# Kernel tuning notes

Measured on AMD Instinct MI355X. Metric: run time of the kernel, lower is better.

## Reference

```python
import jax, jax.numpy as jnp
import numpy as np

# surrogate-gradient spike (multi-gaussian, standard DH-SNN act_fun_adp constants)
GAMMA, LENS, SCALE, HIGHT = 0.5, 0.5, 6.0, 0.15
B_J0, BETA_ADAPT, VTH = 1.6, 1.8, 1.0
IN_DIM, N1, N2, OUT_DIM, BRANCH = 76, 50, 100, 2, 4
BATCH, SEQ = 256, 1000

def _gauss(x, mu, sigma):
    return jnp.exp(-((x - mu) ** 2) / (2.0 * sigma ** 2)) / (jnp.sqrt(2.0 * jnp.pi) * sigma)

@jax.custom_vjp
def spike_fn(x):
    return (x > 0).astype(x.dtype)

def _spike_fwd(x):
    return spike_fn(x), x

def _spike_bwd(x, g):
    sg = (_gauss(x, 0.0, LENS) * (1.0 + HIGHT)
          - _gauss(x, LENS, SCALE * LENS) * HIGHT
          - _gauss(x, -LENS, SCALE * LENS) * HIGHT)
    return (g * sg * GAMMA,)

spike_fn.defvjp(_spike_fwd, _spike_bwd)

def branch_mask(in_dim, out_dim, branch):
    # each dendritic branch k sees contiguous chunk k of the (input|recurrent) vector
    isize = in_dim + out_dim
    seg = int(np.ceil(isize / branch))
    m = np.zeros((out_dim * branch, isize), np.float32)
    for k in range(branch):
        m[k::branch, k * seg:min((k + 1) * seg, isize)] = 1.0
    return jnp.asarray(m)

def setup_inputs():
    key = jax.random.key(0)
    ks = jax.random.split(key, 12)
    def lin(k, o, i):
        lim = 1.0 / np.sqrt(i)
        kw, kb = jax.random.split(k)
        return (jax.random.uniform(kw, (o, i), jnp.float32, -lim, lim),
                jax.random.uniform(kb, (o,), jnp.float32, -lim, lim))
    W1, b1 = lin(ks[0], N1 * BRANCH, IN_DIM + N1)
    W2, b2 = lin(ks[1], N2 * BRANCH, N1 + N2)
    Wx, bx = lin(ks[2], N2, 2 * N2)
    Wm, bm = lin(ks[3], N2, 2 * N2)
    Wa, ba = lin(ks[4], N2, 2 * N2)
    Wd = jax.random.normal(ks[5], (OUT_DIM, N2), jnp.float32) * np.sqrt(2.0 / (OUT_DIM + N2))
    bd = jnp.zeros((OUT_DIM,), jnp.float32)
    tau_m1 = jax.random.uniform(ks[6], (N1,), jnp.float32, 0.0, 4.0)
    tau_n1 = jax.random.uniform(ks[7], (N1, BRANCH), jnp.float32, 0.0, 4.0)
    tau_m2 = jax.random.uniform(ks[8], (N2,), jnp.float32, 0.0, 4.0)
    tau_n2 = jax.random.uniform(ks[9], (N2, BRANCH), jnp.float32, 0.0, 4.0)
    tau_md = jax.random.uniform(ks[10], (OUT_DIM,), jnp.float32, 0.0, 4.0)
    x = jax.random.normal(ks[11], (BATCH, SEQ, IN_DIM), jnp.float32)
    return dict(x=x, W1=W1, b1=b1, tau_m1=tau_m1, tau_n1=tau_n1,
                W2=W2, b2=b2, tau_m2=tau_m2, tau_n2=tau_n2,
                Wx=Wx, bx=bx, Wm=Wm, bm=bm, Wa=Wa, ba=ba,
                Wd=Wd, bd=bd, tau_md=tau_md)

def _denri_step(xt, mem, spk, d, W, b, tau_m, tau_n, n_out):
    # dendritic spiking neuron (spike_rnn_test_denri_wotanh_R)
    kin = jnp.concatenate([xt, spk], axis=1)                       # [B, in+out]
    beta = jax.nn.sigmoid(tau_n)                                   # [out, branch]
    proj = (kin @ W.T + b).reshape(-1, n_out, BRANCH)              # [B, out, branch]
    d = beta * d + (1.0 - beta) * proj
    alpha = jax.nn.sigmoid(tau_m)
    mem = mem * alpha + (1.0 - alpha) * d.sum(-1) - VTH * spk
    spk = spike_fn(mem - VTH)
    return mem, spk, d

def _liquid_step(xt, mem, spk, bth, Wx, bx, Wm, bm, Wa, ba):
    # liquid time-constant adaptive-threshold cell (SNN_rec_cell, is_rec=True)
    dx = jnp.concatenate([xt, spk], axis=1) @ Wx.T + bx
    tauM = jax.nn.sigmoid(jnp.concatenate([dx, mem], axis=1) @ Wm.T + bm)
    tauA = jax.nn.sigmoid(jnp.concatenate([dx, bth], axis=1) @ Wa.T + ba)
    bth = tauA * bth + (1.0 - tauA) * spk
    B = B_J0 + BETA_ADAPT * bth
    mem = mem * tauM + (1.0 - tauM) * dx - B * spk
    spk = spike_fn(mem - B)
    return mem, spk, bth

def reference(x, W1, b1, tau_m1, tau_n1, W2, b2, tau_m2, tau_n2,
              Wx, bx, Wm, bm, Wa, ba, Wd, bd, tau_md):
    Bsz = x.shape[0]
    W1m = W1 * branch_mask(IN_DIM, N1, BRANCH)
    W2m = W2 * branch_mask(N1, N2, BRANCH)
    alpha_d = jax.nn.sigmoid(tau_md)
    z = lambda *s: jnp.zeros(s, x.dtype)
    carry0 = (z(Bsz, N1), z(Bsz, N1), z(Bsz, N1, BRANCH),
              z(Bsz, N2), z(Bsz, N2), z(Bsz, N2, BRANCH),
              z(Bsz, N2), z(Bsz, N2), jnp.full((Bsz, N2), B_J0, x.dtype),
              z(Bsz, OUT_DIM))

    def step(carry, xt):
        m1, s1, d1, m2, s2, d2, lm, ls, lb, md = carry
        m1, s1, d1 = _denri_step(xt, m1, s1, d1, W1m, b1, tau_m1, tau_n1, N1)
        m2, s2, d2 = _denri_step(s1, m2, s2, d2, W2m, b2, tau_m2, tau_n2, N2)
        # original detaches the liquid hidden tuple every step
        lm, ls, lb = (jax.lax.stop_gradient(t) for t in (lm, ls, lb))
        lm, ls, lb = _liquid_step(s2, lm, ls, lb, Wx, bx, Wm, bm, Wa, ba)
        md = md * alpha_d + (1.0 - alpha_d) * (ls @ Wd.T + bd)    # readout integrator
        return (m1, s1, d1, m2, s2, d2, lm, ls, lb, md), md

    _, md_seq = jax.lax.scan(step, carry0, jnp.swapaxes(x, 0, 1))  # [T, B, OUT]
    return md_seq[1:].sum(axis=0)  # output only accumulated for i > 0
```

## Files before the change

kernel.cpp:

```cpp
#include <hip/hip_runtime.h>
#include <math.h>

#define SEQ 1000
#define IND 76
#define PIDX(i) ((((i)/25)*28) + ((i)%25))

__device__ __forceinline__ float sigf(float v) { return 1.0f / (1.0f + expf(-v)); }

__global__ void pack_w2(const float* __restrict__ W2, float* __restrict__ w2pk) {
    const int i = blockIdx.x * 256 + threadIdx.x;
    if (i >= 400 * 40) return;
    const int r = i / 40, u = i - 40 * r;
    const int col = 38 * (r & 3) + u;
    w2pk[i] = (u < 38 && col < 150) ? W2[r * 150 + col] : 0.f;
}

__global__ void pack_wx(const float* __restrict__ Wx, float* __restrict__ wxpk) {
    const int i = blockIdx.x * 256 + threadIdx.x;
    if (i >= 2 * 200 * 64) return;
    const int p = i / (200 * 64);
    const int rem = i - p * 200 * 64;
    const int s = rem / 64, u = rem - 64 * s;
    const int g = s >> 2, c = s & 3;
    const int j = (u >= 28) ? 1 : 0;
    const int local = u - 28 * j;
    float v = 0.f;
    if (local < 25) {
        const int col = (p == 0 ? 100 : 0) + 25 * c + local;
        v = Wx[(2 * g + j) * 200 + col];
    }
    wxpk[i] = v;
}

__global__ __launch_bounds__(512) void dhsnn_fwd(
    const float* __restrict__ x,
    const float* __restrict__ W1, const float* __restrict__ b1,
    const float* __restrict__ tau_m1, const float* __restrict__ tau_n1,
    const float* __restrict__ b2, const float* __restrict__ tau_m2,
    const float* __restrict__ tau_n2,
    const float* __restrict__ bxp, const float* __restrict__ bm,
    const float* __restrict__ ba,
    const float* __restrict__ Wm, const float* __restrict__ Wa,
    const float* __restrict__ Wd, const float* __restrict__ bd,
    const float* __restrict__ tau_md,
    const float* __restrict__ w2pk, const float* __restrict__ wxpk,
    float* __restrict__ out)
{
    const int t   = (int)threadIdx.x;
    const int blk = (int)blockIdx.x;

    __shared__ __align__(16) float kin1P[128];
    __shared__ __align__(16) float kin2P[4][40];
    __shared__ __align__(16) float s2P[112];
    __shared__ __align__(16) float dxP[112];
    __shared__ __align__(16) float lsP[112];
    __shared__ __align__(16) float lmP[112];
    __shared__ __align__(16) float lbP[112];
    __shared__ __align__(16) float sEarly[200];
    __shared__ __align__(16) float dxEarly[100];
    __shared__ __align__(16) float rpart[200];
    __shared__ __align__(16) float r2[8];
    __shared__ float b2S[400], bt2S[400], al2S[100], bmS[100], baS[100], bxS[100];
    __shared__ float wdS[200], b1S[200], bt1S[200], al1S[50];

    for (int i = t; i < 128; i += 512) kin1P[i] = 0.f;
    for (int i = t; i < 160; i += 512) (&kin2P[0][0])[i] = 0.f;
    for (int i = t; i < 112; i += 512) { s2P[i]=0.f; dxP[i]=0.f; lsP[i]=0.f; lmP[i]=0.f; lbP[i]=0.f; }
    for (int i = t; i < 200; i += 512) { sEarly[i] = 0.f; rpart[i] = 0.f; }
    for (int i = t; i < 100; i += 512) dxEarly[i] = 0.f;
    if (t < 8) r2[t] = 0.f;
    if (t < 400) { b2S[t] = b2[t]; bt2S[t] = sigf(tau_n2[t]); }
    if (t < 100) { al2S[t] = sigf(tau_m2[t]); bmS[t] = bm[t]; baS[t] = ba[t]; bxS[t] = bxp[t]; }
    if (t < 200) { wdS[t] = Wd[(t < 100 ? 0 : 100) + (t % 100)];
                   b1S[t] = b1[t]; bt1S[t] = sigf(tau_n1[t]); }
    if (t < 50)  al1S[t] = sigf(tau_m1[t]);

    const int c     = t & 3;
    const int lbase = (t & 63) & ~3;

    float wreg[100];
    float pA = 0.f, pB = 0.f, pC = 0.f, pD = 0.f;
    float mA = 0.f, mS = 0.f;
    float4 xq0 = make_float4(0,0,0,0), xq1 = make_float4(0,0,0,0);

    if (t < 400) {
        const bool late = (t >= 200);
        const int  sg   = late ? ((t - 200) >> 2) : (t >> 2);
        const int  colb = (late ? 0 : 100) + 25 * c;
        const int  r0 = 2 * sg, r1 = 2 * sg + 1;
        #pragma unroll
        for (int u = 0; u < 25; ++u) {
            wreg[u]      = Wm[r0 * 200 + colb + u];
            wreg[25 + u] = Wm[r1 * 200 + colb + u];
            wreg[50 + u] = Wa[r0 * 200 + colb + u];
            wreg[75 + u] = Wa[r1 * 200 + colb + u];
        }
    } else if (t < 500) {
        const int m = t - 400;
        const int rA_ = 2 * m, rB_ = 2 * m + 1;
        const int kA = rA_ & 3, kB = rB_ & 3;
        #pragma unroll
        for (int u = 0; u < 32; ++u) {
            const int cA = 32 * kA + u, cB = 32 * kB + u;
            wreg[u]      = (cA < 126) ? W1[rA_ * 126 + cA] : 0.f;
            wreg[32 + u] = (cB < 126) ? W1[rB_ * 126 + cB] : 0.f;
        }
    } else if (t == 508 || t == 509) {
        pC = sigf(tau_md[t - 508]);
        pD = bd[t - 508];
    }

    auto l1_step = [&]() {
        const int m = t - 400;
        const float* a0p = kin1P + 32 * ((2 * m) & 3);
        const float* a1p = kin1P + 32 * ((2 * m + 1) & 3);
        float acc0 = b1S[2 * m], acc1 = b1S[2 * m + 1];
        #pragma unroll
        for (int u4 = 0; u4 < 8; ++u4) {
            const float4 av = *reinterpret_cast<const float4*>(a0p + 4 * u4);
            acc0 = fmaf(wreg[4*u4+0], av.x, acc0); acc0 = fmaf(wreg[4*u4+1], av.y, acc0);
            acc0 = fmaf(wreg[4*u4+2], av.z, acc0); acc0 = fmaf(wreg[4*u4+3], av.w, acc0);
        }
        #pragma unroll
        for (int u4 = 0; u4 < 8; ++u4) {
            const float4 av = *reinterpret_cast<const float4*>(a1p + 4 * u4);
            acc1 = fmaf(wreg[32+4*u4+0], av.x, acc1); acc1 = fmaf(wreg[32+4*u4+1], av.y, acc1);
            acc1 = fmaf(wreg[32+4*u4+2], av.z, acc1); acc1 = fmaf(wreg[32+4*u4+3], av.w, acc1);
        }
        const float b0 = bt1S[2 * m], b1v = bt1S[2 * m + 1];
        pC = b0 * pC + (1.f - b0) * acc0;
        pD = b1v * pD + (1.f - b1v) * acc1;
        const float pCo = __shfl(pC, (t & 63) | 1, 64);
        const float pDo = __shfl(pD, (t & 63) | 1, 64);
        if ((t & 1) == 0) {
            const float sum = ((pC + pD) + pCo) + pDo;
            const float al = al1S[m >> 1];
            mA = al * mA + (1.f - al) * sum - mS;
            mS = (mA - 1.0f > 0.f) ? 1.f : 0.f;
        }
    };

    __syncthreads();
    if (t < 100) lbP[PIDX(t)] = 1.6f;
    if (t >= 500) {
        const int i0 = t - 500;
        const float* xb = x + (size_t)blk * SEQ * IND;
        *reinterpret_cast<float4*>(&kin1P[4 * i0]) =
            *reinterpret_cast<const float4*>(xb + 4 * i0);
        if (i0 < 7)
            *reinterpret_cast<float4*>(&kin1P[4 * (i0 + 12)]) =
                *reinterpret_cast<const float4*>(xb + 4 * (i0 + 12));
    }
    __syncthreads();
    if (t >= 400 && t < 500) l1_step();
    __syncthreads();
    if (t >= 400 && t < 500 && (t & 1) == 0) {
        const int n = (t - 400) >> 1;
        kin1P[76 + n] = mS;
        const int w = (n >= 38) ? 1 : 0;
        kin2P[w][n - 38 * w] = mS;
    }
    if (t >= 500) {
        const int i0 = t - 500;
        const float* xb = x + ((size_t)blk * SEQ + 1) * IND;
        *reinterpret_cast<float4*>(&kin1P[4 * i0]) =
            *reinterpret_cast<const float4*>(xb + 4 * i0);
        if (i0 < 7)
            *reinterpret_cast<float4*>(&kin1P[4 * (i0 + 12)]) =
                *reinterpret_cast<const float4*>(xb + 4 * (i0 + 12));
    }
    __syncthreads();

    for (int j = 0; j < SEQ; ++j) {
        if (t < 400) {
            const float4* wrow = reinterpret_cast<const float4*>(w2pk + t * 40);
            const float* kw = kin2P[c];
            float a0=0.f, a1=0.f, a2=0.f, a3=0.f;
            #pragma unroll
            for (int cc = 0; cc < 10; ++cc) {
                const float4 wv = wrow[cc];
                const float4 av = *reinterpret_cast<const float4*>(kw + 4 * cc);
                a0 = fmaf(wv.x, av.x, a0); a1 = fmaf(wv.y, av.y, a1);
                a2 = fmaf(wv.z, av.z, a2); a3 = fmaf(wv.w, av.w, a3);
            }
            const float proj = b2S[t] + ((a0 + a1) + (a2 + a3));
            const float bt = bt2S[t];
            pA = bt * pA + (1.f - bt) * proj;
            const float d1 = __shfl(pA, lbase + 1, 64);
            const float d2 = __shfl(pA, lbase + 2, 64);
            const float d3 = __shfl(pA, lbase + 3, 64);
            if (c == 0) {
                const int q = t >> 2;
                const float al = al2S[q];
                const float sum = ((pA + d1) + d2) + d3;
                pB = al * pB + (1.f - al) * sum - s2P[PIDX(q)];
                s2P[PIDX(q)] = (pB - 1.0f > 0.f) ? 1.f : 0.f;
            }
        }
        if (t < 200) {
            const int g = t >> 2;
            {
                const float* apM = lmP + 28 * c;
                const float* apA = lbP + 28 * c;
                float P0=0.f, P1=0.f, P2=0.f, P3=0.f;
                #pragma unroll
                for (int u4 = 0; u4 < 6; ++u4) {
                    const float4 am = *reinterpret_cast<const float4*>(apM + 4 * u4);
                    const float4 aa = *reinterpret_cast<const float4*>(apA + 4 * u4);
                    P0 = fmaf(wreg[   4*u4+0], am.x, P0); P0 = fmaf(wreg[   4*u4+1], am.y, P0);
                    P0 = fmaf(wreg[   4*u4+2], am.z, P0); P0 = fmaf(wreg[   4*u4+3], am.w, P0);
                    P1 = fmaf(wreg[25+4*u4+0], am.x, P1); P1 = fmaf(wreg[25+4*u4+1], am.y, P1);
                    P1 = fmaf(wreg[25+4*u4+2], am.z, P1); P1 = fmaf(wreg[25+4*u4+3], am.w, P1);
                    P2 = fmaf(wreg[50+4*u4+0], aa.x, P2); P2 = fmaf(wreg[50+4*u4+1], aa.y, P2);
                    P2 = fmaf(wreg[50+4*u4+2], aa.z, P2); P2 = fmaf(wreg[50+4*u4+3], aa.w, P2);
                    P3 = fmaf(wreg[75+4*u4+0], aa.x, P3); P3 = fmaf(wreg[75+4*u4+1], aa.y, P3);
                    P3 = fmaf(wreg[75+4*u4+2], aa.z, P3); P3 = fmaf(wreg[75+4*u4+3], aa.w, P3);
                }
                P0 = fmaf(wreg[24], apM[24], P0); P1 = fmaf(wreg[49], apM[24], P1);
                P2 = fmaf(wreg[74], apA[24], P2); P3 = fmaf(wreg[99], apA[24], P3);
                float Q0 = P0 + __shfl_xor(P0, 1, 64), Q1 = P1 + __shfl_xor(P1, 1, 64);
                float Q2 = P2 + __shfl_xor(P2, 1, 64), Q3 = P3 + __shfl_xor(P3, 1, 64);
                float R0 = Q0 + __shfl_xor(Q0, 2, 64), R1 = Q1 + __shfl_xor(Q1, 2, 64);
                float R2 = Q2 + __shfl_xor(Q2, 2, 64), R3 = Q3 + __shfl_xor(Q3, 2, 64);
                sEarly[t] = (c == 0) ? R0 : (c == 1) ? R1 : (c == 2) ? R2 : R3;
            }
            {
                const float* wE = wxpk + (size_t)t * 64;
                const float* aq = lsP + 28 * c;
                float f0 = 0.f, f1 = 0.f;
                #pragma unroll
                for (int u4 = 0; u4 < 6; ++u4) {
                    const float4 w0v = *reinterpret_cast<const float4*>(wE + 4 * u4);
                    const float4 w1v = *reinterpret_cast<const float4*>(wE + 28 + 4 * u4);
                    const float4 av  = *reinterpret_cast<const float4*>(aq + 4 * u4);
                    f0 = fmaf(w0v.x, av.x, f0); f0 = fmaf(w0v.y, av.y, f0);
                    f0 = fmaf(w0v.z, av.z, f0); f0 = fmaf(w0v.w, av.w, f0);
                    f1 = fmaf(w1v.x, av.x, f1); f1 = fmaf(w1v.y, av.y, f1);
                    f1 = fmaf(w1v.z, av.z, f1); f1 = fmaf(w1v.w, av.w, f1);
                }
                f0 = fmaf(wE[24], aq[24], f0);
                f1 = fmaf(wE[52], aq[24], f1);
                float Qf0 = f0 + __shfl_xor(f0, 1, 64), Qf1 = f1 + __shfl_xor(f1, 1, 64);
                float Rf0 = Qf0 + __shfl_xor(Qf0, 2, 64), Rf1 = Qf1 + __shfl_xor(Qf1, 2, 64);
                if (c == 0) dxEarly[2 * g] = Rf0;
                else if (c == 1) dxEarly[2 * g + 1] = Rf1;
            }
            rpart[t] = wdS[t] * lsP[PIDX(t - (t < 100 ? 0 : 100))];
        } else if (t >= 400 && t < 500) {
            if (j < SEQ - 1) l1_step();
        } else if (t >= 500) {
            if (j + 2 < SEQ) {
                const int i0 = t - 500;
                const float* xb = x + ((size_t)blk * SEQ + (j + 2)) * IND;
                xq0 = *reinterpret_cast<const float4*>(xb + 4 * i0);
                if (i0 < 7) xq1 = *reinterpret_cast<const float4*>(xb + 4 * (i0 + 12));
            }
        }
        __syncthreads();
        if (t >= 200 && t < 400) {
            const int s = t - 200, g = s >> 2;
            const float* wL = wxpk + (size_t)(200 + s) * 64;
            const float* aq = s2P + 28 * c;
            float f0 = 0.f, f1 = 0.f;
            #pragma unroll
            for (int u4 = 0; u4 < 6; ++u4) {
                const float4 w0v = *reinterpret_cast<const float4*>(wL + 4 * u4);
                const float4 w1v = *reinterpret_cast<const float4*>(wL + 28 + 4 * u4);
                const float4 av  = *reinterpret_cast<const float4*>(aq + 4 * u4);
                f0 = fmaf(w0v.x, av.x, f0); f0 = fmaf(w0v.y, av.y, f0);
                f0 = fmaf(w0v.z, av.z, f0); f0 = fmaf(w0v.w, av.w, f0);
                f1 = fmaf(w1v.x, av.x, f1); f1 = fmaf(w1v.y, av.y, f1);
                f1 = fmaf(w1v.z, av.z, f1); f1 = fmaf(w1v.w, av.w, f1);
            }
            f0 = fmaf(wL[24], aq[24], f0);
            f1 = fmaf(wL[52], aq[24], f1);
            float Qf0 = f0 + __shfl_xor(f0, 1, 64), Qf1 = f1 + __shfl_xor(f1, 1, 64);
            float Rf0 = Qf0 + __shfl_xor(Qf0, 2, 64), Rf1 = Qf1 + __shfl_xor(Qf1, 2, 64);
            if (c == 0)      dxP[PIDX(2 * g)]     = (Rf0 + dxEarly[2 * g])     + bxS[2 * g];
            else if (c == 1) dxP[PIDX(2 * g + 1)] = (Rf1 + dxEarly[2 * g + 1]) + bxS[2 * g + 1];
        } else if (t < 200) {
            if (c == 0) {
                const int q = t >> 2;
                const int col = 50 + q;
                const int w = (col >= 114) ? 3 : ((col >= 76) ? 2 : 1);
                kin2P[w][col - 38 * w] = s2P[PIDX(q)];
            }
        } else if (t >= 500) {
            if (t < 508) {
                const int rr = t - 500;
                float sV = 0.f;
                #pragma unroll
                for (int u = 0; u < 25; ++u) sV += rpart[25 * rr + u];
                r2[rr] = sV;
            }
            if (j + 2 < SEQ) {
                const int i0 = t - 500;
                *reinterpret_cast<float4*>(&kin1P[4 * i0]) = xq0;
                if (i0 < 7) *reinterpret_cast<float4*>(&kin1P[4 * (i0 + 12)]) = xq1;
            }
        }
        if (t >= 200 && t < 400 && c == 0) {
            const int q = t >> 2;
            const int col = 50 + q;
            const int w = (col >= 114) ? 3 : ((col >= 76) ? 2 : 1);
            kin2P[w][col - 38 * w] = s2P[PIDX(q)];
        }
        __syncthreads();
        if (t >= 200 && t < 400) {
            const int s = t - 200, g = s >> 2;
            const float* apD = dxP + 28 * c;
            float P0=0.f, P1=0.f, P2=0.f, P3=0.f;
            #pragma unroll
            for (int u4 = 0; u4 < 6; ++u4) {
                const float4 ad = *reinterpret_cast<const float4*>(apD + 4 * u4);
                P0 = fmaf(wreg[   4*u4+0], ad.x, P0); P0 = fmaf(wreg[   4*u4+1], ad.y, P0);
                P0 = fmaf(wreg[   4*u4+2], ad.z, P0); P0 = fmaf(wreg[   4*u4+3], ad.w, P0);
                P1 = fmaf(wreg[25+4*u4+0], ad.x, P1); P1 = fmaf(wreg[25+4*u4+1], ad.y, P1);
                P1 = fmaf(wreg[25+4*u4+2], ad.z, P1); P1 = fmaf(wreg[25+4*u4+3], ad.w, P1);
                P2 = fmaf(wreg[50+4*u4+0], ad.x, P2); P2 = fmaf(wreg[50+4*u4+1], ad.y, P2);
                P2 = fmaf(wreg[50+4*u4+2], ad.z, P2); P2 = fmaf(wreg[50+4*u4+3], ad.w, P2);
                P3 = fmaf(wreg[75+4*u4+0], ad.x, P3); P3 = fmaf(wreg[75+4*u4+1], ad.y, P3);
                P3 = fmaf(wreg[75+4*u4+2], ad.z, P3); P3 = fmaf(wreg[75+4*u4+3], ad.w, P3);
            }
            P0 = fmaf(wreg[24], apD[24], P0); P1 = fmaf(wreg[49], apD[24], P1);
            P2 = fmaf(wreg[74], apD[24], P2); P3 = fmaf(wreg[99], apD[24], P3);
            float Q0 = P0 + __shfl_xor(P0, 1, 64), Q1 = P1 + __shfl_xor(P1, 1, 64);
            float Q2 = P2 + __shfl_xor(P2, 1, 64), Q3 = P3 + __shfl_xor(P3, 1, 64);
            float R0 = Q0 + __shfl_xor(Q0, 2, 64), R1 = Q1 + __shfl_xor(Q1, 2, 64);
            float R2 = Q2 + __shfl_xor(Q2, 2, 64), R3 = Q3 + __shfl_xor(Q3, 2, 64);
            const float sel  = (c == 0) ? R0 : (c == 1) ? R1 : (c == 2) ? R2 : R3;
            const float bias = (c < 2) ? bmS[2 * g + c] : baS[2 * g + c - 2];
            const float tv = sigf((sel + sEarly[s]) + bias);
            const float taP = __shfl(tv, lbase + 2 + (c & 1), 64);
            if (c < 2) {
                const int rq = 2 * g + c;
                const float lm = lmP[PIDX(rq)], lb = lbP[PIDX(rq)];
                const float ls = lsP[PIDX(rq)], dxv = dxP[PIDX(rq)];
                const float lbN = taP * lb + (1.f - taP) * ls;
                const float Bv  = 1.6f + 1.8f * lbN;
                const float lmN = lm * tv + (1.f - tv) * dxv - Bv * ls;
                const float lsN = (lmN - Bv > 0.f) ? 1.f : 0.f;
                lmP[PIDX(rq)] = lmN; lbP[PIDX(rq)] = lbN; lsP[PIDX(rq)] = lsN;
            }
        } else if (t >= 400 && t < 500) {
            if ((t & 1) == 0 && j < SEQ - 1) {
                const int n = (t - 400) >> 1;
                kin1P[76 + n] = mS;
                const int w = (n >= 38) ? 1 : 0;
                kin2P[w][n - 38 * w] = mS;
            }
        } else if ((t == 508 || t == 509) && j >= 1) {
            const int o = t - 508;
            const float dot = ((r2[4*o] + r2[4*o+1]) + (r2[4*o+2] + r2[4*o+3])) + pD;
            mA = pC * mA + (1.f - pC) * dot;
            if (j >= 2) mS += mA;
        }
        __syncthreads();
    }

    if (t < 200) rpart[t] = wdS[t] * lsP[PIDX(t - (t < 100 ? 0 : 100))];
    __syncthreads();
    if (t >= 500 && t < 508) {
        const int rr = t - 500;
        float sV = 0.f;
        #pragma unroll
        for (int u = 0; u < 25; ++u) sV += rpart[25 * rr + u];
        r2[rr] = sV;
    }
    __syncthreads();
    if (t == 508 || t == 509) {
        const int o = t - 508;
        const float dot = ((r2[4*o] + r2[4*o+1]) + (r2[4*o+2] + r2[4*o+3])) + pD;
        mA = pC * mA + (1.f - pC) * dot;
        mS += mA;
        out[blk * 2 + o] = mS;
    }
}

extern "C" void kernel_launch(void* const* d_in, const int* in_sizes, int n_in,
                              void* d_out, int out_size, void* d_ws, size_t ws_size,
                              hipStream_t stream) {
    const float* x      = (const float*)d_in[0];
    const float* W1     = (const float*)d_in[1];
    const float* b1     = (const float*)d_in[2];
    const float* tau_m1 = (const float*)d_in[3];
    const float* tau_n1 = (const float*)d_in[4];
    const float* W2     = (const float*)d_in[5];
    const float* b2     = (const float*)d_in[6];
    const float* tau_m2 = (const float*)d_in[7];
    const float* tau_n2 = (const float*)d_in[8];
    const float* Wx     = (const float*)d_in[9];
    const float* bx     = (const float*)d_in[10];
    const float* Wm     = (const float*)d_in[11];
    const float* bm     = (const float*)d_in[12];
    const float* Wa     = (const float*)d_in[13];
    const float* ba     = (const float*)d_in[14];
    const float* Wd     = (const float*)d_in[15];
    const float* bd     = (const float*)d_in[16];
    const float* tau_md = (const float*)d_in[17];
    float* out  = (float*)d_out;
    float* w2pk = (float*)d_ws;
    float* wxpk = (float*)d_ws + 16000;

    pack_w2<<<(400 * 40 + 255) / 256, 256, 0, stream>>>(W2, w2pk);
    pack_wx<<<(2 * 200 * 64 + 255) / 256, 256, 0, stream>>>(Wx, wxpk);

    const int batch = in_sizes[0] / (SEQ * IND);
    dhsnn_fwd<<<batch, 512, 0, stream>>>(x, W1, b1, tau_m1, tau_n1,
                                         b2, tau_m2, tau_n2,
                                         bx, bm, ba, Wm, Wa,
                                         Wd, bd, tau_md,
                                         w2pk, wxpk, out);
}
```

Before: 4.713 ms.

## Software-pipeline layer-2 with double-buffered inputs to cut per-step barriers

Double-buffers the layer-1 and layer-2 input vectors so layer 2 runs one step ahead on 200 threads (two rows each), overlapping with the liquid-layer update. Both Wx partial products (early and late) now run in one phase, and the readout reduction is done with wave shuffles instead of a shared r2 buffer. Together these drop each timestep from three barriers to two, shortening the serial critical path. The cost is more per-thread work for the layer-2 threads and more intricate buffer-parity logic, which could introduce off-by-one timing errors.

```diff
diff --git a/kernel.cpp b/kernel.cpp
--- a/kernel.cpp
+++ b/kernel.cpp
@@ -49,38 +49,33 @@
     const int t   = (int)threadIdx.x;
     const int blk = (int)blockIdx.x;
 
-    __shared__ __align__(16) float kin1P[128];
-    __shared__ __align__(16) float kin2P[4][40];
+    __shared__ __align__(16) float kin1B[2][128];
+    __shared__ __align__(16) float kin2B[2][4][40];
     __shared__ __align__(16) float s2P[112];
     __shared__ __align__(16) float dxP[112];
     __shared__ __align__(16) float lsP[112];
     __shared__ __align__(16) float lmP[112];
     __shared__ __align__(16) float lbP[112];
     __shared__ __align__(16) float sEarly[200];
-    __shared__ __align__(16) float dxEarly[100];
     __shared__ __align__(16) float rpart[200];
-    __shared__ __align__(16) float r2[8];
     __shared__ float b2S[400], bt2S[400], al2S[100], bmS[100], baS[100], bxS[100];
     __shared__ float wdS[200], b1S[200], bt1S[200], al1S[50];
 
-    for (int i = t; i < 128; i += 512) kin1P[i] = 0.f;
-    for (int i = t; i < 160; i += 512) (&kin2P[0][0])[i] = 0.f;
+    for (int i = t; i < 256; i += 512) (&kin1B[0][0])[i] = 0.f;
+    for (int i = t; i < 320; i += 512) (&kin2B[0][0][0])[i] = 0.f;
     for (int i = t; i < 112; i += 512) { s2P[i]=0.f; dxP[i]=0.f; lsP[i]=0.f; lmP[i]=0.f; lbP[i]=0.f; }
     for (int i = t; i < 200; i += 512) { sEarly[i] = 0.f; rpart[i] = 0.f; }
-    for (int i = t; i < 100; i += 512) dxEarly[i] = 0.f;
-    if (t < 8) r2[t] = 0.f;
     if (t < 400) { b2S[t] = b2[t]; bt2S[t] = sigf(tau_n2[t]); }
     if (t < 100) { al2S[t] = sigf(tau_m2[t]); bmS[t] = bm[t]; baS[t] = ba[t]; bxS[t] = bxp[t]; }
     if (t < 200) { wdS[t] = Wd[(t < 100 ? 0 : 100) + (t % 100)];
                    b1S[t] = b1[t]; bt1S[t] = sigf(tau_n1[t]); }
     if (t < 50)  al1S[t] = sigf(tau_m1[t]);
 
-    const int c     = t & 3;
-    const int lbase = (t & 63) & ~3;
+    const int c = t & 3;
 
     float wreg[100];
-    float pA = 0.f, pB = 0.f, pC = 0.f, pD = 0.f;
-    float mA = 0.f, mS = 0.f;
+    float pA = 0.f, pB = 0.f, pD = 0.f, pS = 0.f;
+    float mdA = 0.f, mdB = 0.f;
     float4 xq0 = make_float4(0,0,0,0), xq1 = make_float4(0,0,0,0);
 
     if (t < 400) {
@@ -106,14 +101,14 @@
             wreg[32 + u] = (cB < 126) ? W1[rB_ * 126 + cB] : 0.f;
         }
     } else if (t == 508 || t == 509) {
-        pC = sigf(tau_md[t - 508]);
-        pD = bd[t - 508];
-    }
-
-    auto l1_step = [&]() {
+        mdA = sigf(tau_md[t - 508]);
+        mdB = bd[t - 508];
+    }
+
+    auto l1_step = [&](int p) {
         const int m = t - 400;
-        const float* a0p = kin1P + 32 * ((2 * m) & 3);
-        const float* a1p = kin1P + 32 * ((2 * m + 1) & 3);
+        const float* a0p = kin1B[p] + 32 * ((2 * m) & 3);
+        const float* a1p = kin1B[p] + 32 * ((2 * m + 1) & 3);
         float acc0 = b1S[2 * m], acc1 = b1S[2 * m + 1];
         #pragma unroll
         for (int u4 = 0; u4 < 8; ++u4) {
@@ -128,15 +123,65 @@
             acc1 = fmaf(wreg[32+4*u4+2], av.z, acc1); acc1 = fmaf(wreg[32+4*u4+3], av.w, acc1);
         }
         const float b0 = bt1S[2 * m], b1v = bt1S[2 * m + 1];
-        pC = b0 * pC + (1.f - b0) * acc0;
+        pA = b0 * pA + (1.f - b0) * acc0;
         pD = b1v * pD + (1.f - b1v) * acc1;
-        const float pCo = __shfl(pC, (t & 63) | 1, 64);
+        const float pAo = __shfl(pA, (t & 63) | 1, 64);
         const float pDo = __shfl(pD, (t & 63) | 1, 64);
         if ((t & 1) == 0) {
-            const float sum = ((pC + pD) + pCo) + pDo;
+            const float sum = ((pA + pD) + pAo) + pDo;
             const float al = al1S[m >> 1];
-            mA = al * mA + (1.f - al) * sum - mS;
-            mS = (mA - 1.0f > 0.f) ? 1.f : 0.f;
+            pB = al * pB + (1.f - al) * sum - pS;
+            pS = (pB - 1.0f > 0.f) ? 1.f : 0.f;
+        }
+    };
+    auto s1_write = [&](int pk1, int pk2) {
+        const int n = (t - 400) >> 1;
+        kin1B[pk1][76 + n] = pS;
+        const int w = (n >= 38) ? 1 : 0;
+        kin2B[pk2][w][n - 38 * w] = pS;
+    };
+
+    auto l2_step = [&](int p, int p2) {
+        const int r0 = 2 * t, r1 = r0 + 1;
+        const float4* w0 = reinterpret_cast<const float4*>(w2pk + r0 * 40);
+        const float4* w1 = reinterpret_cast<const float4*>(w2pk + r1 * 40);
+        const float* k0 = kin2B[p][r0 & 3];
+        const float* k1 = kin2B[p][r1 & 3];
+        float a0=0.f, a1=0.f, a2=0.f, a3=0.f;
+        #pragma unroll
+        for (int cc = 0; cc < 10; ++cc) {
+            const float4 wv = w0[cc];
+            const float4 av = *reinterpret_cast<const float4*>(k0 + 4 * cc);
+            a0 = fmaf(wv.x, av.x, a0); a1 = fmaf(wv.y, av.y, a1);
+            a2 = fmaf(wv.z, av.z, a2); a3 = fmaf(wv.w, av.w, a3);
+        }
+        __builtin_amdgcn_sched_barrier(0);
+        float b0=0.f, b1v=0.f, b2v=0.f, b3=0.f;
+        #pragma unroll
+        for (int cc = 0; cc < 10; ++cc) {
+            const float4 wv = w1[cc];
+            const float4 av = *reinterpret_cast<const float4*>(k1 + 4 * cc);
+            b0 = fmaf(wv.x, av.x, b0); b1v = fmaf(wv.y, av.y, b1v);
+            b2v = fmaf(wv.z, av.z, b2v); b3 = fmaf(wv.w, av.w, b3);
+        }
+        const float proj0 = b2S[r0] + ((a0 + a1) + (a2 + a3));
+        const float bt0 = bt2S[r0];
+        pA = bt0 * pA + (1.f - bt0) * proj0;
+        const float proj1 = b2S[r1] + ((b0 + b1v) + (b2v + b3));
+        const float bt1v = bt2S[r1];
+        pD = bt1v * pD + (1.f - bt1v) * proj1;
+        const float sA = __shfl(pA, (t & 63) | 1, 64);
+        const float sD = __shfl(pD, (t & 63) | 1, 64);
+        if ((t & 1) == 0) {
+            const int q = t >> 1;
+            const float sum = ((pA + pD) + sA) + sD;
+            const float al = al2S[q];
+            pB = al * pB + (1.f - al) * sum - s2P[PIDX(q)];
+            const float s2n = (pB - 1.0f > 0.f) ? 1.f : 0.f;
+            s2P[PIDX(q)] = s2n;
+            const int col = 50 + q;
+            const int w = (col >= 114) ? 3 : ((col >= 76) ? 2 : 1);
+            kin2B[p2][w][col - 38 * w] = s2n;
         }
     };
 
@@ -145,61 +190,34 @@
     if (t >= 500) {
         const int i0 = t - 500;
         const float* xb = x + (size_t)blk * SEQ * IND;
-        *reinterpret_cast<float4*>(&kin1P[4 * i0]) =
+        *reinterpret_cast<float4*>(&kin1B[0][4 * i0]) =
             *reinterpret_cast<const float4*>(xb + 4 * i0);
         if (i0 < 7)
-            *reinterpret_cast<float4*>(&kin1P[4 * (i0 + 12)]) =
+            *reinterpret_cast<float4*>(&kin1B[0][4 * (i0 + 12)]) =
                 *reinterpret_cast<const float4*>(xb + 4 * (i0 + 12));
     }
     __syncthreads();
-    if (t >= 400 && t < 500) l1_step();
-    __syncthreads();
-    if (t >= 400 && t < 500 && (t & 1) == 0) {
-        const int n = (t - 400) >> 1;
-        kin1P[76 + n] = mS;
-        const int w = (n >= 38) ? 1 : 0;
-        kin2P[w][n - 38 * w] = mS;
-    }
-    if (t >= 500) {
+    if (t >= 400 && t < 500) {
+        l1_step(0);
+        if ((t & 1) == 0) s1_write(1, 0);
+    } else if (t >= 500) {
         const int i0 = t - 500;
         const float* xb = x + ((size_t)blk * SEQ + 1) * IND;
-        *reinterpret_cast<float4*>(&kin1P[4 * i0]) =
+        *reinterpret_cast<float4*>(&kin1B[1][4 * i0]) =
             *reinterpret_cast<const float4*>(xb + 4 * i0);
         if (i0 < 7)
-            *reinterpret_cast<float4*>(&kin1P[4 * (i0 + 12)]) =
+            *reinterpret_cast<float4*>(&kin1B[1][4 * (i0 + 12)]) =
                 *reinterpret_cast<const float4*>(xb + 4 * (i0 + 12));
     }
     __syncthreads();
+    if (t < 200) l2_step(0, 1);
+    __syncthreads();
 
     for (int j = 0; j < SEQ; ++j) {
-        if (t < 400) {
-            const float4* wrow = reinterpret_cast<const float4*>(w2pk + t * 40);
-            const float* kw = kin2P[c];
-            float a0=0.f, a1=0.f, a2=0.f, a3=0.f;
-            #pragma unroll
-            for (int cc = 0; cc < 10; ++cc) {
-                const float4 wv = wrow[cc];
-                const float4 av = *reinterpret_cast<const float4*>(kw + 4 * cc);
-                a0 = fmaf(wv.x, av.x, a0); a1 = fmaf(wv.y, av.y, a1);
-                a2 = fmaf(wv.z, av.z, a2); a3 = fmaf(wv.w, av.w, a3);
-            }
-            const float proj = b2S[t] + ((a0 + a1) + (a2 + a3));
-            const float bt = bt2S[t];
-            pA = bt * pA + (1.f - bt) * proj;
-            const float d1 = __shfl(pA, lbase + 1, 64);
-            const float d2 = __shfl(pA, lbase + 2, 64);
-            const float d3 = __shfl(pA, lbase + 3, 64);
-            if (c == 0) {
-                const int q = t >> 2;
-                const float al = al2S[q];
-                const float sum = ((pA + d1) + d2) + d3;
-                pB = al * pB + (1.f - al) * sum - s2P[PIDX(q)];
-                s2P[PIDX(q)] = (pB - 1.0f > 0.f) ? 1.f : 0.f;
-            }
-        }
+        const int pj1 = (j + 1) & 1, pj0 = j & 1;
         if (t < 200) {
-            const int g = t >> 2;
             {
+                const int g = t >> 2;  (void)g;
                 const float* apM = lmP + 28 * c;
                 const float* apA = lbP + 28 * c;
                 float P0=0.f, P1=0.f, P2=0.f, P3=0.f;
@@ -224,31 +242,52 @@
                 float R2 = Q2 + __shfl_xor(Q2, 2, 64), R3 = Q3 + __shfl_xor(Q3, 2, 64);
                 sEarly[t] = (c == 0) ? R0 : (c == 1) ? R1 : (c == 2) ? R2 : R3;
             }
-            {
-                const float* wE = wxpk + (size_t)t * 64;
-                const float* aq = lsP + 28 * c;
-                float f0 = 0.f, f1 = 0.f;
-                #pragma unroll
-                for (int u4 = 0; u4 < 6; ++u4) {
-                    const float4 w0v = *reinterpret_cast<const float4*>(wE + 4 * u4);
-                    const float4 w1v = *reinterpret_cast<const float4*>(wE + 28 + 4 * u4);
-                    const float4 av  = *reinterpret_cast<const float4*>(aq + 4 * u4);
-                    f0 = fmaf(w0v.x, av.x, f0); f0 = fmaf(w0v.y, av.y, f0);
-                    f0 = fmaf(w0v.z, av.z, f0); f0 = fmaf(w0v.w, av.w, f0);
-                    f1 = fmaf(w1v.x, av.x, f1); f1 = fmaf(w1v.y, av.y, f1);
-                    f1 = fmaf(w1v.z, av.z, f1); f1 = fmaf(w1v.w, av.w, f1);
-                }
-                f0 = fmaf(wE[24], aq[24], f0);
-                f1 = fmaf(wE[52], aq[24], f1);
-                float Qf0 = f0 + __shfl_xor(f0, 1, 64), Qf1 = f1 + __shfl_xor(f1, 1, 64);
-                float Rf0 = Qf0 + __shfl_xor(Qf0, 2, 64), Rf1 = Qf1 + __shfl_xor(Qf1, 2, 64);
-                if (c == 0) dxEarly[2 * g] = Rf0;
-                else if (c == 1) dxEarly[2 * g + 1] = Rf1;
-            }
-            rpart[t] = wdS[t] * lsP[PIDX(t - (t < 100 ? 0 : 100))];
-        } else if (t >= 400 && t < 500) {
-            if (j < SEQ - 1) l1_step();
-        } else if (t >= 500) {
+            rpart[t] = wdS[t] * lsP[PIDX(t % 100)];
+        } else if (t < 400) {
+            const int s = t - 200, g = s >> 2;
+            const float* wEp = wxpk + (size_t)s * 64;
+            const float* wLp = wxpk + (size_t)(200 + s) * 64;
+            const float* aE = lsP + 28 * c;
+            const float* aL = s2P + 28 * c;
+            float e0=0.f, e1=0.f;
+            #pragma unroll
+            for (int u4 = 0; u4 < 6; ++u4) {
+                const float4 w0v = *reinterpret_cast<const float4*>(wEp + 4 * u4);
+                const float4 w1v = *reinterpret_cast<const float4*>(wEp + 28 + 4 * u4);
+                const float4 av  = *reinterpret_cast<const float4*>(aE + 4 * u4);
+                e0 = fmaf(w0v.x, av.x, e0); e0 = fmaf(w0v.y, av.y, e0);
+                e0 = fmaf(w0v.z, av.z, e0); e0 = fmaf(w0v.w, av.w, e0);
+                e1 = fmaf(w1v.x, av.x, e1); e1 = fmaf(w1v.y, av.y, e1);
+                e1 = fmaf(w1v.z, av.z, e1); e1 = fmaf(w1v.w, av.w, e1);
+            }
+            e0 = fmaf(wEp[24], aE[24], e0);
+            e1 = fmaf(wEp[52], aE[24], e1);
+            __builtin_amdgcn_sched_barrier(0);
+            float l0=0.f, l1v=0.f;
+            #pragma unroll
+            for (int u4 = 0; u4 < 6; ++u4) {
+                const float4 w0v = *reinterpret_cast<const float4*>(wLp + 4 * u4);
+                const float4 w1v = *reinterpret_cast<const float4*>(wLp + 28 + 4 * u4);
+                const float4 av  = *reinterpret_cast<const float4*>(aL + 4 * u4);
+                l0 = fmaf(w0v.x, av.x, l0); l0 = fmaf(w0v.y, av.y, l0);
+                l0 = fmaf(w0v.z, av.z, l0); l0 = fmaf(w0v.w, av.w, l0);
+                l1v = fmaf(w1v.x, av.x, l1v); l1v = fmaf(w1v.y, av.y, l1v);
+                l1v = fmaf(w1v.z, av.z, l1v); l1v = fmaf(w1v.w, av.w, l1v);
+            }
+            l0  = fmaf(wLp[24], aL[24], l0);
+            l1v = fmaf(wLp[52], aL[24], l1v);
+            float QE0 = e0 + __shfl_xor(e0, 1, 64), QE1 = e1 + __shfl_xor(e1, 1, 64);
+            float RE0 = QE0 + __shfl_xor(QE0, 2, 64), RE1 = QE1 + __shfl_xor(QE1, 2, 64);
+            float QL0 = l0 + __shfl_xor(l0, 1, 64), QL1 = l1v + __shfl_xor(l1v, 1, 64);
+            float RL0 = QL0 + __shfl_xor(QL0, 2, 64), RL1 = QL1 + __shfl_xor(QL1, 2, 64);
+            if (c == 0)      dxP[PIDX(2*g)]   = (RL0 + RE0) + bxS[2*g];
+            else if (c == 1) dxP[PIDX(2*g+1)] = (RL1 + RE1) + bxS[2*g+1];
+        } else if (t < 500) {
+            if (j < SEQ - 1) {
+                l1_step(pj1);
+                if ((t & 1) == 0) s1_write(pj0, pj1);
+            }
+        } else {
             if (j + 2 < SEQ) {
                 const int i0 = t - 500;
                 const float* xb = x + ((size_t)blk * SEQ + (j + 2)) * IND;
@@ -257,56 +296,9 @@
             }
         }
         __syncthreads();
-        if (t >= 200 && t < 400) {
-            const int s = t - 200, g = s >> 2;
-            const float* wL = wxpk + (size_t)(200 + s) * 64;
-            const float* aq = s2P + 28 * c;
-            float f0 = 0.f, f1 = 0.f;
-            #pragma unroll
-            for (int u4 = 0; u4 < 6; ++u4) {
-                const float4 w0v = *reinterpret_cast<const float4*>(wL + 4 * u4);
-                const float4 w1v = *reinterpret_cast<const float4*>(wL + 28 + 4 * u4);
-                const float4 av  = *reinterpret_cast<const float4*>(aq + 4 * u4);
-                f0 = fmaf(w0v.x, av.x, f0); f0 = fmaf(w0v.y, av.y, f0);
-                f0 = fmaf(w0v.z, av.z, f0); f0 = fmaf(w0v.w, av.w, f0);
-                f1 = fmaf(w1v.x, av.x, f1); f1 = fmaf(w1v.y, av.y, f1);
-                f1 = fmaf(w1v.z, av.z, f1); f1 = fmaf(w1v.w, av.w, f1);
-            }
-            f0 = fmaf(wL[24], aq[24], f0);
-            f1 = fmaf(wL[52], aq[24], f1);
-            float Qf0 = f0 + __shfl_xor(f0, 1, 64), Qf1 = f1 + __shfl_xor(f1, 1, 64);
-            float Rf0 = Qf0 + __shfl_xor(Qf0, 2, 64), Rf1 = Qf1 + __shfl_xor(Qf1, 2, 64);
-            if (c == 0)      dxP[PIDX(2 * g)]     = (Rf0 + dxEarly[2 * g])     + bxS[2 * g];
-            else if (c == 1) dxP[PIDX(2 * g + 1)] = (Rf1 + dxEarly[2 * g + 1]) + bxS[2 * g + 1];
-        } else if (t < 200) {
-            if (c == 0) {
-                const int q = t >> 2;
-                const int col = 50 + q;
-                const int w = (col >= 114) ? 3 : ((col >= 76) ? 2 : 1);
-                kin2P[w][col - 38 * w] = s2P[PIDX(q)];
-            }
-        } else if (t >= 500) {
-            if (t < 508) {
-                const int rr = t - 500;
-                float sV = 0.f;
-                #pragma unroll
-                for (int u = 0; u < 25; ++u) sV += rpart[25 * rr + u];
-                r2[rr] = sV;
-            }
-            if (j + 2 < SEQ) {
-                const int i0 = t - 500;
-                *reinterpret_cast<float4*>(&kin1P[4 * i0]) = xq0;
-                if (i0 < 7) *reinterpret_cast<float4*>(&kin1P[4 * (i0 + 12)]) = xq1;
-            }
-        }
-        if (t >= 200 && t < 400 && c == 0) {
-            const int q = t >> 2;
-            const int col = 50 + q;
-            const int w = (col >= 114) ? 3 : ((col >= 76) ? 2 : 1);
-            kin2P[w][col - 38 * w] = s2P[PIDX(q)];
-        }
-        __syncthreads();
-        if (t >= 200 && t < 400) {
+        if (t < 200) {
+            if (j < SEQ - 1) l2_step(pj1, pj0);
+        } else if (t < 400) {
             const int s = t - 200, g = s >> 2;
             const float* apD = dxP + 28 * c;
             float P0=0.f, P1=0.f, P2=0.f, P3=0.f;
@@ -329,11 +321,12 @@
             float R0 = Q0 + __shfl_xor(Q0, 2, 64), R1 = Q1 + __shfl_xor(Q1, 2, 64);
             float R2 = Q2 + __shfl_xor(Q2, 2, 64), R3 = Q3 + __shfl_xor(Q3, 2, 64);
             const float sel  = (c == 0) ? R0 : (c == 1) ? R1 : (c == 2) ? R2 : R3;
-            const float bias = (c < 2) ? bmS[2 * g + c] : baS[2 * g + c - 2];
+            const float bias = (c < 2) ? bmS[2*g + c] : baS[2*g + c - 2];
             const float tv = sigf((sel + sEarly[s]) + bias);
+            const int lbase = (t & 63) & ~3;
             const float taP = __shfl(tv, lbase + 2 + (c & 1), 64);
             if (c < 2) {
-                const int rq = 2 * g + c;
+                const int rq = 2*g + c;
                 const float lm = lmP[PIDX(rq)], lb = lbP[PIDX(rq)];
                 const float ls = lsP[PIDX(rq)], dxv = dxP[PIDX(rq)];
                 const float lbN = taP * lb + (1.f - taP) * ls;
@@ -342,38 +335,52 @@
                 const float lsN = (lmN - Bv > 0.f) ? 1.f : 0.f;
                 lmP[PIDX(rq)] = lmN; lbP[PIDX(rq)] = lbN; lsP[PIDX(rq)] = lsN;
             }
-        } else if (t >= 400 && t < 500) {
-            if ((t & 1) == 0 && j < SEQ - 1) {
-                const int n = (t - 400) >> 1;
-                kin1P[76 + n] = mS;
-                const int w = (n >= 38) ? 1 : 0;
-                kin2P[w][n - 38 * w] = mS;
-            }
-        } else if ((t == 508 || t == 509) && j >= 1) {
+        } else if (t >= 500) {
+            if (j + 2 < SEQ) {
+                const int i0 = t - 500;
+                *reinterpret_cast<float4*>(&kin1B[pj0][4 * i0]) = xq0;
+                if (i0 < 7) *reinterpret_cast<float4*>(&kin1B[pj0][4 * (i0 + 12)]) = xq1;
+            }
+            const int rr = t - 500;
+            const int rrc = (rr < 8) ? rr : 7;
+            float sV = 0.f;
+            #pragma unroll
+            for (int u = 0; u < 25; ++u) sV += rpart[25 * rrc + u];
             const int o = t - 508;
-            const float dot = ((r2[4*o] + r2[4*o+1]) + (r2[4*o+2] + r2[4*o+3])) + pD;
-            mA = pC * mA + (1.f - pC) * dot;
-            if (j >= 2) mS += mA;
+            const int sb = 52 + 4 * ((o == 1) ? 1 : 0);
+            const float v0 = __shfl(sV, sb + 0, 64);
+            const float v1 = __shfl(sV, sb + 1, 64);
+            const float v2 = __shfl(sV, sb + 2, 64);
+            const float v3 = __shfl(sV, sb + 3, 64);
+            if ((t == 508 || t == 509) && j >= 1) {
+                const float dot = ((v0 + v1) + (v2 + v3)) + mdB;
+                pA = mdA * pA + (1.f - mdA) * dot;
+                if (j >= 2) pB += pA;
+            }
         }
         __syncthreads();
     }
 
-    if (t < 200) rpart[t] = wdS[t] * lsP[PIDX(t - (t < 100 ? 0 : 100))];
+    if (t < 200) rpart[t] = wdS[t] * lsP[PIDX(t % 100)];
     __syncthreads();
-    if (t >= 500 && t < 508) {
+    if (t >= 500) {
         const int rr = t - 500;
+        const int rrc = (rr < 8) ? rr : 7;
         float sV = 0.f;
         #pragma unroll
-        for (int u = 0; u < 25; ++u) sV += rpart[25 * rr + u];
-        r2[rr] = sV;
-    }
-    __syncthreads();
-    if (t == 508 || t == 509) {
+        for (int u = 0; u < 25; ++u) sV += rpart[25 * rrc + u];
         const int o = t - 508;
-        const float dot = ((r2[4*o] + r2[4*o+1]) + (r2[4*o+2] + r2[4*o+3])) + pD;
-        mA = pC * mA + (1.f - pC) * dot;
-        mS += mA;
-        out[blk * 2 + o] = mS;
+        const int sb = 52 + 4 * ((o == 1) ? 1 : 0);
+        const float v0 = __shfl(sV, sb + 0, 64);
+        const float v1 = __shfl(sV, sb + 1, 64);
+        const float v2 = __shfl(sV, sb + 2, 64);
+        const float v3 = __shfl(sV, sb + 3, 64);
+        if (t == 508 || t == 509) {
+            const float dot = ((v0 + v1) + (v2 + v3)) + mdB;
+            pA = mdA * pA + (1.f - mdA) * dot;
+            pB += pA;
+            out[blk * 2 + (t - 508)] = pB;
+        }
     }
 }
 
```

New measurement: 6.769 ms. 43.6% more time.
